# Kernel optimization log

Hardware: AMD Instinct MI355X
Metric: run time of the kernel (lower is better)

Reference implementation:

```python
import jax, jax.numpy as jnp
import numpy as np

HIDDEN = 2048
NUM_HEADS = 32
NUM_KV_HEADS = 8
HEAD_DIM = 64
ROPE_THETA = 10000.0


def _rope_tables(S, dtype=jnp.float32):
    freqs = 1.0 / (ROPE_THETA ** (jnp.arange(0, HEAD_DIM, 2, dtype=jnp.float32) / HEAD_DIM))
    angles = jnp.arange(S, dtype=jnp.float32)[:, None] * freqs[None, :]  # [S, D/2]
    return jnp.cos(angles).astype(dtype), jnp.sin(angles).astype(dtype)


def _apply_rope(x, cos, sin):
    # x: [B, H, S, D] with interleaved even/odd rotation pairs
    xe = x[..., 0::2]
    xo = x[..., 1::2]
    oe = xe * cos - xo * sin
    oo = xe * sin + xo * cos
    return jnp.stack([oe, oo], axis=-1).reshape(x.shape)


def setup_inputs() -> dict:
    key = jax.random.key(0)
    ks = jax.random.split(key, 5)
    scale = 0.02
    return {
        "x": jax.random.normal(ks[0], (2, 2048, HIDDEN), dtype=jnp.float32),
        "wq": jax.random.normal(ks[1], (NUM_HEADS * HEAD_DIM, HIDDEN), dtype=jnp.float32) * scale,
        "wk": jax.random.normal(ks[2], (NUM_KV_HEADS * HEAD_DIM, HIDDEN), dtype=jnp.float32) * scale,
        "wv": jax.random.normal(ks[3], (NUM_KV_HEADS * HEAD_DIM, HIDDEN), dtype=jnp.float32) * scale,
        "wo": jax.random.normal(ks[4], (HIDDEN, NUM_HEADS * HEAD_DIM), dtype=jnp.float32) * scale,
    }


def reference(x, wq, wk, wv, wo):
    B, S, _ = x.shape
    G = NUM_HEADS // NUM_KV_HEADS  # GQA group size

    q = (x @ wq.T).reshape(B, S, NUM_HEADS, HEAD_DIM).transpose(0, 2, 1, 3)      # [B,Hq,S,D]
    k = (x @ wk.T).reshape(B, S, NUM_KV_HEADS, HEAD_DIM).transpose(0, 2, 1, 3)   # [B,Hkv,S,D]
    v = (x @ wv.T).reshape(B, S, NUM_KV_HEADS, HEAD_DIM).transpose(0, 2, 1, 3)

    cos, sin = _rope_tables(S, x.dtype)
    q = _apply_rope(q, cos, sin)
    k = _apply_rope(k, cos, sin)

    # GQA without materializing repeated K/V: fold group dim into q
    qg = q.reshape(B, NUM_KV_HEADS, G, S, HEAD_DIM)
    scale = 1.0 / jnp.sqrt(jnp.asarray(HEAD_DIM, dtype=x.dtype))
    scores = jnp.einsum("bkgsd,bktd->bkgst", qg, k) * scale  # [B,Hkv,G,S,S]

    causal = jnp.tril(jnp.ones((S, S), dtype=bool))
    scores = jnp.where(causal, scores, jnp.finfo(scores.dtype).min)
    probs = jax.nn.softmax(scores, axis=-1)

    out = jnp.einsum("bkgst,bktd->bkgsd", probs, v)                 # [B,Hkv,G,S,D]
    out = out.reshape(B, NUM_HEADS, S, HEAD_DIM).transpose(0, 2, 1, 3).reshape(B, S, NUM_HEADS * HEAD_DIM)
    return out @ wo.T
```

## Files before the change

### kernel.cpp

```cpp
#include <hip/hip_runtime.h>
#include <hip/hip_bf16.h>

typedef __hip_bfloat16 bf16;
typedef __attribute__((ext_vector_type(8))) short short8;
typedef __attribute__((ext_vector_type(4))) float f32x4;

#define S_LEN 2048
#define BATCH 2
#define M_TOT 4096
#define HID 2048
#define NH 32
#define NKV 8
#define HD 64
#define KVD 512
#define QSCALE 0.125f

#define MFMA16(a, b, c) __builtin_amdgcn_mfma_f32_16x16x32_bf16(a, b, c, 0, 0, 0)

__device__ __forceinline__ void gload_lds16(const bf16* g, bf16* l) {
    __builtin_amdgcn_global_load_lds((const __attribute__((address_space(1))) void*)g,
                                     (__attribute__((address_space(3))) void*)l,
                                     16, 0, 0);
}

__device__ __forceinline__ float b2f(short v) {
    unsigned u = ((unsigned)(unsigned short)v) << 16;
    float f; __builtin_memcpy(&f, &u, 4); return f;
}

#define N8_X   1048576
#define N8_WQ   524288
#define N8_WK   131072
#define N8_TOT 2359296
#define NTBL   65536
__global__ void cast_all_kernel(const float* __restrict__ x, const float* __restrict__ wq,
                                const float* __restrict__ wk, const float* __restrict__ wv,
                                const float* __restrict__ wo, bf16* __restrict__ dst,
                                float* __restrict__ cosb, float* __restrict__ sinb) {
    int stride = gridDim.x * blockDim.x;
    for (int i = blockIdx.x * blockDim.x + threadIdx.x; i < N8_TOT + NTBL; i += stride) {
        if (i >= N8_TOT) {
            int idx = i - N8_TOT;
            int s = idx >> 5, d = idx & 31;
            float freq = powf(10000.0f, -(float)(2 * d) / 64.0f);
            float ang = (float)s * freq;
            cosb[idx] = cosf(ang);
            sinb[idx] = sinf(ang);
            continue;
        }
        const float* s; int off;
        if (i < N8_X)                        { s = x;  off = i; }
        else if (i < N8_X + N8_WQ)           { s = wq; off = i - N8_X; }
        else if (i < N8_X + N8_WQ + N8_WK)   { s = wk; off = i - (N8_X + N8_WQ); }
        else if (i < N8_X + N8_WQ + 2*N8_WK) { s = wv; off = i - (N8_X + N8_WQ + N8_WK); }
        else                                 { s = wo; off = i - (N8_X + N8_WQ + 2*N8_WK); }
        const float4* sp = (const float4*)(s + (size_t)off * 8);
        float4 a = sp[0], b = sp[1];
        bf16 tmp[8];
        tmp[0] = __float2bfloat16(a.x); tmp[1] = __float2bfloat16(a.y);
        tmp[2] = __float2bfloat16(a.z); tmp[3] = __float2bfloat16(a.w);
        tmp[4] = __float2bfloat16(b.x); tmp[5] = __float2bfloat16(b.y);
        tmp[6] = __float2bfloat16(b.z); tmp[7] = __float2bfloat16(b.w);
        *(short8*)(dst + (size_t)i * 8) = *(short8*)tmp;
    }
}

__device__ __forceinline__ short8 rope8(short8 v, float4 c, float4 s, float scale) {
    short8 o;
    const float* cp = (const float*)&c;
    const float* sp = (const float*)&s;
    #pragma unroll
    for (int m = 0; m < 4; m++) {
        float xe = b2f(v[2 * m]) * scale;
        float xo = b2f(v[2 * m + 1]) * scale;
        bf16 oe = __float2bfloat16(xe * cp[m] - xo * sp[m]);
        bf16 oo = __float2bfloat16(xe * sp[m] + xo * cp[m]);
        short se, so;
        __builtin_memcpy(&se, &oe, 2); __builtin_memcpy(&so, &oo, 2);
        o[2 * m] = se; o[2 * m + 1] = so;
    }
    return o;
}

__device__ __forceinline__ void gemm_core(const bf16* __restrict__ A,
                                          const bf16* __restrict__ W,
                                          int K, int m0, int n0,
                                          bf16* As, bf16* Bs,
                                          f32x4 acc[4][4]) {
    int tid = threadIdx.x;
    int lane = tid & 63, wid = tid >> 6;
    int wr = wid >> 1, wc = wid & 1;
    int lhi = lane >> 4, llo = lane & 15;
    int c0 = tid, c1 = tid + 256;
    int r0 = c0 >> 2, s0 = ((c0 & 3) ^ ((r0 >> 1) & 3)) * 8;
    int r1 = c1 >> 2, s1 = ((c1 & 3) ^ ((r1 >> 1) & 3)) * 8;
    const bf16* gA0 = A + (size_t)(m0 + r0) * K + s0;
    const bf16* gA1 = A + (size_t)(m0 + r1) * K + s1;
    const bf16* gB0 = W + (size_t)(n0 + r0) * K + s0;
    const bf16* gB1 = W + (size_t)(n0 + r1) * K + s1;

    auto stage = [&](int buf, int k0) {
        bf16* a = As + buf * 4096;
        bf16* b = Bs + buf * 4096;
        gload_lds16(gA0 + k0, a + c0 * 8);
        gload_lds16(gA1 + k0, a + c1 * 8);
        gload_lds16(gB0 + k0, b + c0 * 8);
        gload_lds16(gB1 + k0, b + c1 * 8);
    };
    auto compute = [&](int buf) {
        const bf16* Ac = As + buf * 4096;
        const bf16* Bc = Bs + buf * 4096;
        short8 af[4], bfr[4];
        #pragma unroll
        for (int i = 0; i < 4; i++) {
            int row = wr * 64 + i * 16 + llo;
            af[i] = *(const short8*)(Ac + row * 32 + ((lhi ^ ((row >> 1) & 3)) * 8));
        }
        #pragma unroll
        for (int j = 0; j < 4; j++) {
            int row = wc * 64 + j * 16 + llo;
            bfr[j] = *(const short8*)(Bc + row * 32 + ((lhi ^ ((row >> 1) & 3)) * 8));
        }
        __builtin_amdgcn_s_setprio(1);
        #pragma unroll
        for (int i = 0; i < 4; i++)
            #pragma unroll
            for (int j = 0; j < 4; j++)
                acc[i][j] = MFMA16(af[i], bfr[j], acc[i][j]);
        __builtin_amdgcn_s_setprio(0);
    };

    int nt = K / 32;
    stage(0, 0);
    stage(1, 32);
    int b0 = 0, b1 = 1, b2 = 2;
    for (int t = 0; t < nt - 1; ++t) {
        asm volatile("s_waitcnt vmcnt(4)" ::: "memory");
        __builtin_amdgcn_s_barrier();
        if (t + 2 < nt) stage(b2, (t + 2) * 32);
        __builtin_amdgcn_sched_barrier(0);
        compute(b0);
        int tmp = b0; b0 = b1; b1 = b2; b2 = tmp;
    }
    asm volatile("s_waitcnt vmcnt(0)" ::: "memory");
    __builtin_amdgcn_s_barrier();
    compute(b0);
}

__global__ __launch_bounds__(256) void gemm_qkv_kernel(
        const bf16* __restrict__ xb,
        const bf16* __restrict__ wq, const bf16* __restrict__ wk, const bf16* __restrict__ wv,
        const float* __restrict__ cosb, const float* __restrict__ sinb,
        bf16* __restrict__ qb, bf16* __restrict__ kb, bf16* __restrict__ vtb) {
    __shared__ bf16 As[3 * 128 * 32];
    __shared__ bf16 Bs[3 * 128 * 32];
    int by = blockIdx.y;
    const bf16* W; bf16* Cb; int n0, ldc, mode;
    if (by < 16)      { W = wq; Cb = qb;  n0 = by * 128;        ldc = 2048; mode = 0; }
    else if (by < 20) { W = wk; Cb = kb;  n0 = (by - 16) * 128; ldc = 512;  mode = 2; }
    else              { W = wv; Cb = vtb; n0 = (by - 20) * 128; ldc = 0;    mode = 1; }
    int bx = blockIdx.x;
    int bxs = (bx & 7) * 4 + (bx >> 3);
    int m0 = bxs * 128;

    f32x4 acc[4][4] = {};
    gemm_core(xb, W, HID, m0, n0, As, Bs, acc);

    int lane = threadIdx.x & 63, wid = threadIdx.x >> 6;
    int wr = wid >> 1, wc = wid & 1;
    int lhi = lane >> 4, llo = lane & 15;
    #pragma unroll
    for (int i = 0; i < 4; i++)
        #pragma unroll
        for (int j = 0; j < 4; j++) {
            int col = wc * 64 + j * 16 + llo;
            #pragma unroll
            for (int r = 0; r < 4; r++) {
                int row = wr * 64 + i * 16 + lhi * 4 + r;
                int m = m0 + row;
                float v = acc[i][j][r];
                if (mode == 0) {
                    Cb[(size_t)m * ldc + n0 + col] = __float2bfloat16(v);
                } else if (mode == 1) {
                    int bb = m >> 11, ss = m & 2047;
                    Cb[((size_t)(bb * 512 + n0 + col)) * S_LEN + ss] = __float2bfloat16(v);
                } else {
                    int dcol = n0 + col;
                    int dd = dcol & 63;
                    int pidx = dd >> 1;
                    float sgn = (dd & 1) ? 1.0f : -1.0f;
                    int ss = m & 2047;
                    float c  = cosb[ss * 32 + pidx];
                    float sn = sinb[ss * 32 + pidx];
                    float o = __shfl_xor(v, 1, 64);
                    float outv = v * c + sgn * o * sn;
                    Cb[(size_t)m * 512 + dcol] = __float2bfloat16(outv);
                }
            }
        }
}

__global__ __launch_bounds__(256) void gemm_out_kernel(
        const bf16* __restrict__ attnb, const bf16* __restrict__ wob,
        float* __restrict__ out) {
    __shared__ bf16 As[3 * 128 * 32];
    __shared__ bf16 Bs[3 * 128 * 32];
    int bx = blockIdx.x;
    int bxs = (bx & 7) * 4 + (bx >> 3);
    int m0 = bxs * 128;
    int n0 = blockIdx.y * 128;
    f32x4 acc[4][4] = {};
    gemm_core(attnb, wob, HID, m0, n0, As, Bs, acc);

    int lane = threadIdx.x & 63, wid = threadIdx.x >> 6;
    int wr = wid >> 1, wc = wid & 1;
    int lhi = lane >> 4, llo = lane & 15;
    #pragma unroll
    for (int i = 0; i < 4; i++)
        #pragma unroll
        for (int j = 0; j < 4; j++) {
            int col = wc * 64 + j * 16 + llo;
            #pragma unroll
            for (int r = 0; r < 4; r++) {
                int row = wr * 64 + i * 16 + lhi * 4 + r;
                out[(size_t)(m0 + row) * HID + n0 + col] = acc[i][j][r];
            }
        }
}

__global__ __launch_bounds__(256, 4) void flash_kernel(
        const bf16* __restrict__ qb, const bf16* __restrict__ kb,
        const bf16* __restrict__ vtb, const float* __restrict__ cosb,
        const float* __restrict__ sinb, bf16* __restrict__ attnb) {
    __shared__ bf16 Ks[2][64 * 64];
    __shared__ bf16 Vs[2][64 * 64];
    __shared__ bf16 Pl[4][16 * 64];
    int bh = blockIdx.y;
    int b = bh >> 5, h = bh & 31;
    int kvh = h >> 2;
    int tid = threadIdx.x;
    int wid = tid >> 6, lane = tid & 63;
    int lhi = lane >> 4, llo = lane & 15;

    const bf16* Kg = kb + (size_t)(b * S_LEN) * KVD + kvh * HD;
    const bf16* Vg = vtb + (size_t)(b * 512 + kvh * 64) * S_LEN;

    int c0 = tid, c1 = tid + 256;
    int r0 = c0 >> 3, s0 = ((c0 & 7) ^ (r0 & 7)) * 8;
    int r1 = c1 >> 3, s1 = ((c1 & 7) ^ (r1 & 7)) * 8;

    bf16* pl = &Pl[wid][0];
    const int xw = llo & 7;
    const int hh = lhi >> 1;
    bf16* pwb = pl + llo * 64 + (lhi & 1) * 4;
    const int prd0 = llo * 64 + ((lhi ^ xw) * 8);
    const int prd1 = llo * 64 + (((lhi + 4) ^ xw) * 8);

    auto stage = [&](int buf, int t0) {
        gload_lds16(Kg + (size_t)(t0 + r0) * KVD + s0, &Ks[buf][c0 * 8]);
        gload_lds16(Kg + (size_t)(t0 + r1) * KVD + s1, &Ks[buf][c1 * 8]);
        gload_lds16(Vg + (size_t)r0 * S_LEN + t0 + s0, &Vs[buf][c0 * 8]);
        gload_lds16(Vg + (size_t)r1 * S_LEN + t0 + s1, &Vs[buf][c1 * 8]);
    };

    auto run_phase = [&](int j) {
        int qrow0 = j * 64 + wid * 16;
        int spos = qrow0 + llo;
        const bf16* qrow = qb + ((size_t)(b * S_LEN) + spos) * (NH * HD) + h * HD;
        float4 cv0 = *(const float4*)(cosb + spos * 32 + lhi * 4);
        float4 sv0 = *(const float4*)(sinb + spos * 32 + lhi * 4);
        float4 cv1 = *(const float4*)(cosb + spos * 32 + 16 + lhi * 4);
        float4 sv1 = *(const float4*)(sinb + spos * 32 + 16 + lhi * 4);
        short8 qf0 = rope8(*(const short8*)(qrow + lhi * 8), cv0, sv0, QSCALE);
        short8 qf1 = rope8(*(const short8*)(qrow + 32 + lhi * 8), cv1, sv1, QSCALE);

        f32x4 acc[4] = {};
        float psum = 0.f;
        int qloc = wid * 16 + llo;

        stage(0, 0);
        asm volatile("s_waitcnt vmcnt(0)" ::: "memory");
        __builtin_amdgcn_s_barrier();
        int cur = 0;
        for (int t = 0; t <= j; ++t) {
            int t0 = t * 64;
            if (t < j) stage(cur ^ 1, t0 + 64);
            const bf16* Kc = &Ks[cur][0];
            const bf16* Vc = &Vs[cur][0];
            f32x4 z[4];
            __builtin_amdgcn_s_setprio(1);
            #pragma unroll
            for (int cb = 0; cb < 4; cb++) {
                int row = cb * 16 + llo;
                short8 k0 = *(const short8*)(Kc + row * 64 + ((lhi ^ xw) * 8));
                short8 k1 = *(const short8*)(Kc + row * 64 + (((lhi + 4) ^ xw) * 8));
                f32x4 zz = {0.f, 0.f, 0.f, 0.f};
                zz = MFMA16(k0, qf0, zz);
                zz = MFMA16(k1, qf1, zz);
                z[cb] = zz;
            }
            __builtin_amdgcn_s_setprio(0);
            bool diag = (t == j);
            #pragma unroll
            for (int cb = 0; cb < 4; cb++) {
                float p0 = __expf(z[cb][0]);
                float p1 = __expf(z[cb][1]);
                float p2 = __expf(z[cb][2]);
                float p3 = __expf(z[cb][3]);
                if (diag) {
                    int kl = cb * 16 + lhi * 4;
                    p0 = (kl + 0 <= qloc) ? p0 : 0.f;
                    p1 = (kl + 1 <= qloc) ? p1 : 0.f;
                    p2 = (kl + 2 <= qloc) ? p2 : 0.f;
                    p3 = (kl + 3 <= qloc) ? p3 : 0.f;
                }
                psum += (p0 + p1) + (p2 + p3);
                bf16 tmp[4];
                tmp[0] = __float2bfloat16(p0); tmp[1] = __float2bfloat16(p1);
                tmp[2] = __float2bfloat16(p2); tmp[3] = __float2bfloat16(p3);
                *(uint2*)(pwb + (((2 * cb + hh) ^ xw) * 8)) = *(uint2*)tmp;
            }
            short8 pa0 = *(const short8*)(pl + prd0);
            short8 pa1 = *(const short8*)(pl + prd1);
            __builtin_amdgcn_s_setprio(1);
            #pragma unroll
            for (int jb = 0; jb < 4; jb++) {
                int row = jb * 16 + llo;
                short8 v0 = *(const short8*)(Vc + row * 64 + ((lhi ^ xw) * 8));
                short8 v1 = *(const short8*)(Vc + row * 64 + (((lhi + 4) ^ xw) * 8));
                acc[jb] = MFMA16(pa0, v0, acc[jb]);
                acc[jb] = MFMA16(pa1, v1, acc[jb]);
            }
            __builtin_amdgcn_s_setprio(0);
            asm volatile("s_waitcnt vmcnt(0)" ::: "memory");
            __builtin_amdgcn_s_barrier();
            cur ^= 1;
        }
        psum += __shfl_xor(psum, 16, 64);
        psum += __shfl_xor(psum, 32, 64);
        float inv[4];
        #pragma unroll
        for (int r = 0; r < 4; r++)
            inv[r] = 1.0f / __shfl(psum, lhi * 4 + r, 64);
        size_t obase = ((size_t)(b * S_LEN) + qrow0) * (NH * HD) + h * HD;
        #pragma unroll
        for (int jb = 0; jb < 4; jb++)
            #pragma unroll
            for (int r = 0; r < 4; r++)
                attnb[obase + (size_t)(lhi * 4 + r) * (NH * HD) + jb * 16 + llo] =
                    __float2bfloat16(acc[jb][r] * inv[r]);
    };

    run_phase(blockIdx.x);
    run_phase(31 - blockIdx.x);
}

extern "C" void kernel_launch(void* const* d_in, const int* in_sizes, int n_in,
                              void* d_out, int out_size, void* d_ws, size_t ws_size,
                              hipStream_t stream) {
    const float* x  = (const float*)d_in[0];
    const float* wq = (const float*)d_in[1];
    const float* wk = (const float*)d_in[2];
    const float* wv = (const float*)d_in[3];
    const float* wo = (const float*)d_in[4];
    float* out = (float*)d_out;

    char* ws = (char*)d_ws;
    size_t off = 0;
    auto alloc = [&](size_t bytes) { void* p = ws + off; off += (bytes + 255) & ~(size_t)255; return p; };
    bf16* xb   = (bf16*)alloc((size_t)M_TOT * HID * 2);
    bf16* wqb  = (bf16*)alloc((size_t)HID * HID * 2);
    bf16* wkb  = (bf16*)alloc((size_t)512 * HID * 2);
    bf16* wvb  = (bf16*)alloc((size_t)512 * HID * 2);
    bf16* wob  = (bf16*)alloc((size_t)HID * HID * 2);
    bf16* qb   = (bf16*)alloc((size_t)M_TOT * 2048 * 2);
    bf16* kb   = (bf16*)alloc((size_t)M_TOT * 512 * 2);
    bf16* vtb  = (bf16*)alloc((size_t)M_TOT * 512 * 2);
    bf16* attnb= (bf16*)alloc((size_t)M_TOT * 2048 * 2);
    float* cosb= (float*)alloc((size_t)S_LEN * 32 * 4);
    float* sinb= (float*)alloc((size_t)S_LEN * 32 * 4);

    cast_all_kernel<<<2048, 256, 0, stream>>>(x, wq, wk, wv, wo, xb, cosb, sinb);

    gemm_qkv_kernel<<<dim3(M_TOT / 128, 24), 256, 0, stream>>>(xb, wqb, wkb, wvb,
                                                               cosb, sinb, qb, kb, vtb);

    flash_kernel<<<dim3(16, BATCH * NH), 256, 0, stream>>>(qb, kb, vtb, cosb, sinb, attnb);

    gemm_out_kernel<<<dim3(M_TOT / 128, HID / 128), 256, 0, stream>>>(attnb, wob, out);
}
```

Before: 191.5 us.

## Split flash attention tile 2x2 across waves over queries and keys

Each wave now handles 32 query rows against half of the 64 keys in a tile, instead of 16 query rows against all 64 keys. Every K and V fragment loaded from LDS now feeds two MFMAs, which cuts LDS read traffic per MFMA. The two key-half partial outputs and row sums are combined at the end through LDS scratch that reuses the K/V buffers, adding two block barriers per phase. Register pressure also rises because each wave now holds twice the accumulators.

```diff
diff --git a/kernel.cpp b/kernel.cpp
--- a/kernel.cpp
+++ b/kernel.cpp
@@ -234,13 +234,14 @@
         const float* __restrict__ sinb, bf16* __restrict__ attnb) {
     __shared__ bf16 Ks[2][64 * 64];
     __shared__ bf16 Vs[2][64 * 64];
-    __shared__ bf16 Pl[4][16 * 64];
+    __shared__ bf16 Pl[4][1024];
     int bh = blockIdx.y;
     int b = bh >> 5, h = bh & 31;
     int kvh = h >> 2;
     int tid = threadIdx.x;
     int wid = tid >> 6, lane = tid & 63;
     int lhi = lane >> 4, llo = lane & 15;
+    int wq2 = wid >> 1, wk2 = wid & 1;
 
     const bf16* Kg = kb + (size_t)(b * S_LEN) * KVD + kvh * HD;
     const bf16* Vg = vtb + (size_t)(b * 512 + kvh * 64) * S_LEN;
@@ -250,11 +251,6 @@
     int r1 = c1 >> 3, s1 = ((c1 & 7) ^ (r1 & 7)) * 8;
 
     bf16* pl = &Pl[wid][0];
-    const int xw = llo & 7;
-    const int hh = lhi >> 1;
-    bf16* pwb = pl + llo * 64 + (lhi & 1) * 4;
-    const int prd0 = llo * 64 + ((lhi ^ xw) * 8);
-    const int prd1 = llo * 64 + (((lhi + 4) ^ xw) * 8);
 
     auto stage = [&](int buf, int t0) {
         gload_lds16(Kg + (size_t)(t0 + r0) * KVD + s0, &Ks[buf][c0 * 8]);
@@ -264,19 +260,22 @@
     };
 
     auto run_phase = [&](int j) {
-        int qrow0 = j * 64 + wid * 16;
-        int spos = qrow0 + llo;
-        const bf16* qrow = qb + ((size_t)(b * S_LEN) + spos) * (NH * HD) + h * HD;
-        float4 cv0 = *(const float4*)(cosb + spos * 32 + lhi * 4);
-        float4 sv0 = *(const float4*)(sinb + spos * 32 + lhi * 4);
-        float4 cv1 = *(const float4*)(cosb + spos * 32 + 16 + lhi * 4);
-        float4 sv1 = *(const float4*)(sinb + spos * 32 + 16 + lhi * 4);
-        short8 qf0 = rope8(*(const short8*)(qrow + lhi * 8), cv0, sv0, QSCALE);
-        short8 qf1 = rope8(*(const short8*)(qrow + 32 + lhi * 8), cv1, sv1, QSCALE);
-
-        f32x4 acc[4] = {};
-        float psum = 0.f;
-        int qloc = wid * 16 + llo;
+        int qbase = j * 64 + wq2 * 32;
+        short8 qf[2][2];
+        #pragma unroll
+        for (int qg = 0; qg < 2; qg++) {
+            int spos = qbase + qg * 16 + llo;
+            const bf16* qr = qb + ((size_t)(b * S_LEN) + spos) * (NH * HD) + h * HD;
+            float4 cv0 = *(const float4*)(cosb + spos * 32 + lhi * 4);
+            float4 sv0 = *(const float4*)(sinb + spos * 32 + lhi * 4);
+            float4 cv1 = *(const float4*)(cosb + spos * 32 + 16 + lhi * 4);
+            float4 sv1 = *(const float4*)(sinb + spos * 32 + 16 + lhi * 4);
+            qf[qg][0] = rope8(*(const short8*)(qr + lhi * 8), cv0, sv0, QSCALE);
+            qf[qg][1] = rope8(*(const short8*)(qr + 32 + lhi * 8), cv1, sv1, QSCALE);
+        }
+
+        f32x4 acc[2][4] = {};
+        float psum[2] = {0.f, 0.f};
 
         stage(0, 0);
         asm volatile("s_waitcnt vmcnt(0)" ::: "memory");
@@ -287,68 +286,106 @@
             if (t < j) stage(cur ^ 1, t0 + 64);
             const bf16* Kc = &Ks[cur][0];
             const bf16* Vc = &Vs[cur][0];
-            f32x4 z[4];
+            f32x4 z[2][2];
             __builtin_amdgcn_s_setprio(1);
             #pragma unroll
-            for (int cb = 0; cb < 4; cb++) {
-                int row = cb * 16 + llo;
-                short8 k0 = *(const short8*)(Kc + row * 64 + ((lhi ^ xw) * 8));
-                short8 k1 = *(const short8*)(Kc + row * 64 + (((lhi + 4) ^ xw) * 8));
-                f32x4 zz = {0.f, 0.f, 0.f, 0.f};
-                zz = MFMA16(k0, qf0, zz);
-                zz = MFMA16(k1, qf1, zz);
-                z[cb] = zz;
+            for (int kg = 0; kg < 2; kg++) {
+                int krow = wk2 * 32 + kg * 16 + llo;
+                int x = krow & 7;
+                short8 k0 = *(const short8*)(Kc + krow * 64 + ((lhi ^ x) * 8));
+                short8 k1 = *(const short8*)(Kc + krow * 64 + (((lhi + 4) ^ x) * 8));
+                #pragma unroll
+                for (int qg = 0; qg < 2; qg++) {
+                    f32x4 zz = {0.f, 0.f, 0.f, 0.f};
+                    zz = MFMA16(k0, qf[qg][0], zz);
+                    zz = MFMA16(k1, qf[qg][1], zz);
+                    z[kg][qg] = zz;
+                }
             }
             __builtin_amdgcn_s_setprio(0);
             bool diag = (t == j);
             #pragma unroll
-            for (int cb = 0; cb < 4; cb++) {
-                float p0 = __expf(z[cb][0]);
-                float p1 = __expf(z[cb][1]);
-                float p2 = __expf(z[cb][2]);
-                float p3 = __expf(z[cb][3]);
-                if (diag) {
-                    int kl = cb * 16 + lhi * 4;
-                    p0 = (kl + 0 <= qloc) ? p0 : 0.f;
-                    p1 = (kl + 1 <= qloc) ? p1 : 0.f;
-                    p2 = (kl + 2 <= qloc) ? p2 : 0.f;
-                    p3 = (kl + 3 <= qloc) ? p3 : 0.f;
+            for (int kg = 0; kg < 2; kg++)
+                #pragma unroll
+                for (int qg = 0; qg < 2; qg++) {
+                    float p0 = __expf(z[kg][qg][0]);
+                    float p1 = __expf(z[kg][qg][1]);
+                    float p2 = __expf(z[kg][qg][2]);
+                    float p3 = __expf(z[kg][qg][3]);
+                    if (diag) {
+                        int kl = wk2 * 32 + kg * 16 + lhi * 4;
+                        int ql = wq2 * 32 + qg * 16 + llo;
+                        p0 = (kl + 0 <= ql) ? p0 : 0.f;
+                        p1 = (kl + 1 <= ql) ? p1 : 0.f;
+                        p2 = (kl + 2 <= ql) ? p2 : 0.f;
+                        p3 = (kl + 3 <= ql) ? p3 : 0.f;
+                    }
+                    psum[qg] += (p0 + p1) + (p2 + p3);
+                    bf16 tmp[4];
+                    tmp[0] = __float2bfloat16(p0); tmp[1] = __float2bfloat16(p1);
+                    tmp[2] = __float2bfloat16(p2); tmp[3] = __float2bfloat16(p3);
+                    *(uint2*)(pl + qg * 512 + llo * 32 + kg * 16 + lhi * 4) = *(uint2*)tmp;
                 }
-                psum += (p0 + p1) + (p2 + p3);
-                bf16 tmp[4];
-                tmp[0] = __float2bfloat16(p0); tmp[1] = __float2bfloat16(p1);
-                tmp[2] = __float2bfloat16(p2); tmp[3] = __float2bfloat16(p3);
-                *(uint2*)(pwb + (((2 * cb + hh) ^ xw) * 8)) = *(uint2*)tmp;
-            }
-            short8 pa0 = *(const short8*)(pl + prd0);
-            short8 pa1 = *(const short8*)(pl + prd1);
+            short8 pa0 = *(const short8*)(pl + llo * 32 + lhi * 8);
+            short8 pa1 = *(const short8*)(pl + 512 + llo * 32 + lhi * 8);
             __builtin_amdgcn_s_setprio(1);
             #pragma unroll
-            for (int jb = 0; jb < 4; jb++) {
-                int row = jb * 16 + llo;
-                short8 v0 = *(const short8*)(Vc + row * 64 + ((lhi ^ xw) * 8));
-                short8 v1 = *(const short8*)(Vc + row * 64 + (((lhi + 4) ^ xw) * 8));
-                acc[jb] = MFMA16(pa0, v0, acc[jb]);
-                acc[jb] = MFMA16(pa1, v1, acc[jb]);
+            for (int dg = 0; dg < 4; dg++) {
+                int vrow = dg * 16 + llo;
+                int xv = vrow & 7;
+                short8 vf = *(const short8*)(Vc + vrow * 64 + (((wk2 * 4 + lhi) ^ xv) * 8));
+                acc[0][dg] = MFMA16(pa0, vf, acc[0][dg]);
+                acc[1][dg] = MFMA16(pa1, vf, acc[1][dg]);
             }
             __builtin_amdgcn_s_setprio(0);
             asm volatile("s_waitcnt vmcnt(0)" ::: "memory");
             __builtin_amdgcn_s_barrier();
             cur ^= 1;
         }
-        psum += __shfl_xor(psum, 16, 64);
-        psum += __shfl_xor(psum, 32, 64);
-        float inv[4];
-        #pragma unroll
-        for (int r = 0; r < 4; r++)
-            inv[r] = 1.0f / __shfl(psum, lhi * 4 + r, 64);
-        size_t obase = ((size_t)(b * S_LEN) + qrow0) * (NH * HD) + h * HD;
-        #pragma unroll
-        for (int jb = 0; jb < 4; jb++)
-            #pragma unroll
-            for (int r = 0; r < 4; r++)
-                attnb[obase + (size_t)(lhi * 4 + r) * (NH * HD) + jb * 16 + llo] =
-                    __float2bfloat16(acc[jb][r] * inv[r]);
+        #pragma unroll
+        for (int qg = 0; qg < 2; qg++) {
+            psum[qg] += __shfl_xor(psum[qg], 16, 64);
+            psum[qg] += __shfl_xor(psum[qg], 32, 64);
+        }
+        float* scrO = (float*)&Ks[0][0];
+        float* scrP = (float*)&Vs[0][0];
+        if (wk2 == 1) {
+            #pragma unroll
+            for (int qg = 0; qg < 2; qg++) {
+                #pragma unroll
+                for (int dg = 0; dg < 4; dg++)
+                    #pragma unroll
+                    for (int r = 0; r < 4; r++)
+                        scrO[wq2 * 2048 + (qg * 16 + lhi * 4 + r) * 64 + dg * 16 + llo]
+                            = acc[qg][dg][r];
+                if (lhi == 0) scrP[wq2 * 32 + qg * 16 + llo] = psum[qg];
+            }
+        }
+        __syncthreads();
+        if (wk2 == 0) {
+            size_t obase = ((size_t)(b * S_LEN) + qbase) * (NH * HD) + h * HD;
+            #pragma unroll
+            for (int qg = 0; qg < 2; qg++) {
+                psum[qg] += scrP[wq2 * 32 + qg * 16 + llo];
+                #pragma unroll
+                for (int dg = 0; dg < 4; dg++)
+                    #pragma unroll
+                    for (int r = 0; r < 4; r++)
+                        acc[qg][dg][r] +=
+                            scrO[wq2 * 2048 + (qg * 16 + lhi * 4 + r) * 64 + dg * 16 + llo];
+                float inv[4];
+                #pragma unroll
+                for (int r = 0; r < 4; r++)
+                    inv[r] = 1.0f / __shfl(psum[qg], lhi * 4 + r, 64);
+                #pragma unroll
+                for (int dg = 0; dg < 4; dg++)
+                    #pragma unroll
+                    for (int r = 0; r < 4; r++)
+                        attnb[obase + (size_t)(qg * 16 + lhi * 4 + r) * (NH * HD) + dg * 16 + llo]
+                            = __float2bfloat16(acc[qg][dg][r] * inv[r]);
+            }
+        }
+        __syncthreads();
     };
 
     run_phase(blockIdx.x);
```

Result: slower. 209.5 us (+9.4%).
